# Kernel tuning notes

Hardware: AMD Instinct MI355X
Metric: run time of the kernel (lower is better)

Reference implementation:

```python
import jax, jax.numpy as jnp
import numpy as np

NL, D, Di, N, R, K, V, NH = 24, 768, 1536, 16, 48, 4, 50280, 12
BATCH, SEQ = 4, 256


def setup_inputs():
    key = jax.random.key(0)
    it = iter(jax.random.split(key, 48))
    g = lambda shape, s=0.02: jax.random.normal(next(it), shape, jnp.float32) * s
    inp = {
        "question_ids": jax.random.randint(next(it), (BATCH, SEQ), 0, V),
        "question_mask": jnp.ones((BATCH, SEQ), jnp.int32),
        "answer_ids": jax.random.randint(next(it), (BATCH, SEQ), 0, V),
        "answer_mask": jnp.ones((BATCH, SEQ), jnp.int32),
        "embed": g((V, D)),
        "norm_w": jnp.ones((NL, D)),
        "in_proj_w": g((NL, 2 * Di, D)),
        "conv_w": g((NL, Di, K), 0.1),
        "conv_b": jnp.zeros((NL, Di)),
        "x_proj_w": g((NL, R + 2 * N, Di)),
        "dt_proj_w": g((NL, Di, R)),
        "dt_proj_b": g((NL, Di), 0.5) - 4.0,
        "A_log": jnp.log(jnp.broadcast_to(jnp.arange(1, N + 1, dtype=jnp.float32), (NL, Di, N))) + 0.0,
        "D_p": jnp.ones((NL, Di)),
        "out_proj_w": g((NL, D, Di)),
        "norm_f": jnp.ones((D,)),
        "ln1_w": jnp.ones((D,)), "ln1_b": jnp.zeros((D,)),
        "qkv_w": g((3 * D, D)), "qkv_b": jnp.zeros((3 * D,)),
        "attn_out_w": g((D, D)), "attn_out_b": jnp.zeros((D,)),
        "ln2_w": jnp.ones((D,)), "ln2_b": jnp.zeros((D,)),
        "ff1_w": g((4 * D, D)), "ff1_b": jnp.zeros((4 * D,)),
        "ff2_w": g((D, 4 * D)), "ff2_b": jnp.zeros((D,)),
        "C_w": g((1, N)), "proj_out_w": g((D, Di)),
        "B_w": g((N, 1)), "proj_in_w": g((Di, D), 0.002),
    }
    return inp


def _rms(x, w, eps=1e-5):
    return x * jax.lax.rsqrt(jnp.mean(x * x, axis=-1, keepdims=True) + eps) * w


def _ln(x, w, b, eps=1e-5):
    m = jnp.mean(x, axis=-1, keepdims=True)
    v = jnp.var(x, axis=-1, keepdims=True)
    return (x - m) * jax.lax.rsqrt(v + eps) * w + b


def _mamba_block(h, layer, init_state):
    nw, ipw, cw, cb, xpw, dpw, dpb, alog, dp, opw = layer
    x_in = _rms(h, nw)
    xz = jnp.einsum('bld,ed->ble', x_in, ipw)  # (B,L,2*Di)
    x, z = jnp.split(xz, 2, axis=-1)
    L = x.shape[1]
    xp = jnp.pad(x, ((0, 0), (K - 1, 0), (0, 0)))  # causal depthwise conv, kernel K
    x = sum(xp[:, k:k + L, :] * cw[:, k] for k in range(K)) + cb
    x = jax.nn.silu(x)
    dbl = jnp.einsum('bld,ed->ble', x, xpw)
    dt, Bm, Cm = dbl[..., :R], dbl[..., R:R + N], dbl[..., R + N:]
    delta = jax.nn.softplus(jnp.einsum('blr,dr->bld', dt, dpw) + dpb)  # (B,L,Di)
    A = -jnp.exp(alog)  # (Di,N)

    def step(hs, t):  # selective scan, carry (B,Di,N)
        d_t, x_t, B_t, C_t = t
        hs = jnp.exp(d_t[..., None] * A) * hs + (d_t * x_t)[..., None] * B_t[:, None, :]
        return hs, jnp.einsum('bdn,bn->bd', hs, C_t)

    xs = tuple(jnp.moveaxis(a, 1, 0) for a in (delta, x, Bm, Cm))
    last, ys = jax.lax.scan(step, init_state, xs)
    y = jnp.moveaxis(ys, 0, 1) + x * dp
    y = y * jax.nn.silu(z)
    return h + jnp.einsum('bld,od->blo', y, opw), last


def _backbone(ids, mask, embed, mamba_params, norm_f, init_states):
    h = embed[ids] * mask[..., None].astype(embed.dtype)
    block = jax.checkpoint(_mamba_block)  # remat per layer: bounds bwd memory

    def layer_step(carry, xs):
        *layer, st = xs
        return block(carry, tuple(layer), st)

    h, lasts = jax.lax.scan(layer_step, h, mamba_params + (init_states,))
    h = _rms(h, norm_f)
    return jnp.einsum('bld,vd->blv', h, embed), lasts  # tied lm head


def _tf_layer(x, ln1_w, ln1_b, qkv_w, qkv_b, attn_out_w, attn_out_b, ln2_w, ln2_b, ff1_w, ff1_b, ff2_w, ff2_b):
    B, S, _ = x.shape
    hd = D // NH
    y = _ln(x, ln1_w, ln1_b)  # norm_first pre-LN
    q, k, v = jnp.split(y @ qkv_w.T + qkv_b, 3, axis=-1)
    q = q.reshape(B, S, NH, hd); k = k.reshape(B, S, NH, hd); v = v.reshape(B, S, NH, hd)
    att = jax.nn.softmax(jnp.einsum('bqhd,bkhd->bhqk', q, k) / jnp.sqrt(jnp.float32(hd)), axis=-1)
    o = jnp.einsum('bhqk,bkhd->bqhd', att, v).reshape(B, S, D)
    x = x + o @ attn_out_w.T + attn_out_b
    y = _ln(x, ln2_w, ln2_b)
    return x + jax.nn.gelu(y @ ff1_w.T + ff1_b, approximate=False) @ ff2_w.T + ff2_b


def _refine(states, C_w, proj_out_w, B_w, proj_in_w, tf_params):
    # states: (B, NL, Di, N); 12-step recurrent state refinement
    for _ in range(12):
        d = jnp.einsum('bsdn,n->bsd', states, C_w[0])  # C: Linear(16,1), squeeze(-1)
        d = jnp.einsum('bsd,od->bso', d, proj_out_w)   # 1536 -> 768
        d = _tf_layer(d, *tf_params)
        d = jnp.einsum('bso,do->bsd', d, proj_in_w)    # 768 -> 1536
        states = states + d[..., None] * B_w[:, 0]     # B: Linear(1,16)
    return states


def reference(question_ids, question_mask, answer_ids, answer_mask, embed, norm_w, in_proj_w, conv_w, conv_b, x_proj_w, dt_proj_w, dt_proj_b, A_log, D_p, out_proj_w, norm_f, ln1_w, ln1_b, qkv_w, qkv_b, attn_out_w, attn_out_b, ln2_w, ln2_b, ff1_w, ff1_b, ff2_w, ff2_b, C_w, proj_out_w, B_w, proj_in_w):
    mamba_params = (norm_w, in_proj_w, conv_w, conv_b, x_proj_w, dt_proj_w, dt_proj_b, A_log, D_p, out_proj_w)
    tf_params = (ln1_w, ln1_b, qkv_w, qkv_b, attn_out_w, attn_out_b, ln2_w, ln2_b, ff1_w, ff1_b, ff2_w, ff2_b)
    Bsz = question_ids.shape[0]
    zeros = jnp.zeros((NL, Bsz, Di, N), embed.dtype)
    _, lasts = _backbone(question_ids, question_mask, embed, mamba_params, norm_f, zeros)
    states = jnp.moveaxis(lasts, 0, 1)  # torch.stack(states, dim=1): (B, NL, Di, N)
    states = _refine(states, C_w, proj_out_w, B_w, proj_in_w, tf_params)
    logits, _ = _backbone(answer_ids, answer_mask, embed, mamba_params, norm_f, jnp.moveaxis(states, 0, 1))
    return logits
```

## Files before the change

### kernel.cpp

```cpp
#include <hip/hip_runtime.h>
#include <math.h>

namespace {

constexpr int kNL = 24, kD = 768, kDi = 1536, kN = 16, kR = 48, kK = 4, kV = 50280, kNH = 12;
constexpr int kB = 4, kS = 256;
constexpr int kMtok = kB * kS;
constexpr int kMref = kB * kNL;
constexpr int kVp = 50304;
constexpr int kKa = 3840;

using bf16x8   = __attribute__((ext_vector_type(8))) short;
using f32x4    = __attribute__((ext_vector_type(4))) float;
using ushort8v = __attribute__((ext_vector_type(8))) unsigned short;

__device__ __forceinline__ float siluf(float x) { return x / (1.f + __expf(-x)); }

__device__ __forceinline__ ushort f2b(float f) {
    union { float f; unsigned u; } v; v.f = f;
    unsigned u = v.u;
    unsigned r = (u + 0x7FFFu + ((u >> 16) & 1u)) >> 16;
    return (ushort)r;
}
__device__ __forceinline__ float b2f(ushort u) {
    union { unsigned u; float f; } v; v.u = (unsigned)u << 16; return v.f;
}

#define GLOAD_LDS(g, l) \
    __builtin_amdgcn_global_load_lds((const __attribute__((address_space(1))) void*)(g), \
                                     (__attribute__((address_space(3))) void*)(l), 16, 0, 0)

template <int BM, int BN, int BIAS, int ACT, int RES, int OUTMODE, int PIPE, int SSQ = 0>
__global__ __launch_bounds__(256, (PIPE == 3 ? 3 : 2)) void gemm_bf16(
    const ushort* __restrict__ A, int lda,
    const ushort* __restrict__ B, int ldb,
    float* __restrict__ C, int ldc,
    ushort* __restrict__ Cbf, int ldcb,
    float* __restrict__ C2,
    const float* __restrict__ bias,
    const float* __restrict__ aux,
    const float* __restrict__ aux2,
    int M, int N, int K)
{
    constexpr int ACH = BM / 32;
    constexpr int BCH = BN / 32;
    constexpr int MI  = BM / 32;
    constexpr int NJ  = BN / 32;

    __shared__ ushort As[PIPE][BM * 64];
    __shared__ ushort Bs[PIPE][BN * 64];

    const int tid  = threadIdx.x;
    const int lane = tid & 63;
    const int wave = tid >> 6;
    const int m0 = blockIdx.y * BM;
    const int n0 = blockIdx.x * BN;
    const int wr = (wave >> 1) * (BM / 2);
    const int wc = (wave & 1) * (BN / 2);

    f32x4 acc[MI][NJ];
#pragma unroll
    for (int i = 0; i < MI; ++i)
#pragma unroll
        for (int j = 0; j < NJ; ++j) acc[i][j] = f32x4{0.f, 0.f, 0.f, 0.f};

    const int srow = lane >> 3;
    const int scol = ((lane & 7) ^ srow) * 8;
    const ushort* gA[ACH];
    const ushort* gB[BCH];
#pragma unroll
    for (int g = 0; g < ACH; ++g)
        gA[g] = A + (size_t)(m0 + (g * 4 + wave) * 8 + srow) * lda + scol;
#pragma unroll
    for (int g = 0; g < BCH; ++g)
        gB[g] = B + (size_t)(n0 + (g * 4 + wave) * 8 + srow) * ldb + scol;

    const int frow = lane & 15;
    const int kh   = lane >> 4;
    const int nt   = K >> 6;

    auto stage = [&](int t, int buf) {
        const int off = t * 64;
#pragma unroll
        for (int g = 0; g < ACH; ++g) GLOAD_LDS(gA[g] + off, &As[buf][(g * 4 + wave) * 512]);
#pragma unroll
        for (int g = 0; g < BCH; ++g) GLOAD_LDS(gB[g] + off, &Bs[buf][(g * 4 + wave) * 512]);
    };
    auto compute = [&](int buf) {
#pragma unroll
        for (int s = 0; s < 2; ++s) {
            bf16x8 fa[MI], fb[NJ];
#pragma unroll
            for (int i = 0; i < MI; ++i) {
                int r = wr + i * 16 + frow;
                int slot = (s * 4 + kh) ^ (r & 7);
                fa[i] = *(const bf16x8*)&As[buf][r * 64 + slot * 8];
            }
#pragma unroll
            for (int j = 0; j < NJ; ++j) {
                int r = wc + j * 16 + frow;
                int slot = (s * 4 + kh) ^ (r & 7);
                fb[j] = *(const bf16x8*)&Bs[buf][r * 64 + slot * 8];
            }
#pragma unroll
            for (int i = 0; i < MI; ++i)
#pragma unroll
                for (int j = 0; j < NJ; ++j)
                    acc[i][j] = __builtin_amdgcn_mfma_f32_16x16x32_bf16(fa[i], fb[j], acc[i][j], 0, 0, 0);
        }
    };

    if constexpr (PIPE == 3) {
        stage(0, 0);
        if (nt > 1) stage(1, 1);
        for (int t = 0; t < nt; ++t) {
            if (t < nt - 1) {
                asm volatile("s_waitcnt vmcnt(%0)" :: "n"(ACH + BCH) : "memory");
            } else {
                asm volatile("s_waitcnt vmcnt(0)" ::: "memory");
            }
            __builtin_amdgcn_s_barrier();
            if (t + 2 < nt) stage(t + 2, (t + 2) % 3);
            compute(t % 3);
        }
        __builtin_amdgcn_s_barrier();
    } else {
        stage(0, 0);
        __syncthreads();
        int cur = 0;
        for (int t = 0; t < nt; ++t) {
            if (t + 1 < nt) stage(t + 1, cur ^ 1);
            compute(cur);
            __syncthreads();
            cur ^= 1;
        }
    }

    const int ccol = lane & 15;
    const int crow = (lane >> 4) * 4;
    float rsq[MI][4], rsm[MI][4];
    if constexpr (SSQ) {
#pragma unroll
        for (int i = 0; i < MI; ++i)
#pragma unroll
            for (int q = 0; q < 4; ++q) { rsq[i][q] = 0.f; rsm[i][q] = 0.f; }
    }
#pragma unroll
    for (int i = 0; i < MI; ++i) {
#pragma unroll
        for (int j = 0; j < NJ; ++j) {
            int gn = n0 + wc + j * 16 + ccol;
            if (gn >= N) continue;
            float bv = BIAS ? bias[gn] : 0.f;
#pragma unroll
            for (int q = 0; q < 4; ++q) {
                int gm = m0 + wr + i * 16 + crow + q;
                if (gm >= M) continue;
                float v = acc[i][j][q] + bv;
                if (ACT == 1) v = fmaxf(v, 0.f) + log1pf(expf(-fabsf(v)));
                if (ACT == 2) v = 0.5f * v * (1.f + erff(v * 0.70710678118654752f));
                if (OUTMODE == 3) {
                    if (gn < 48) Cbf[(size_t)gm * 64 + gn] = f2b(v);
                    else if (gn < 64) { Cbf[(size_t)gm * 64 + gn] = 0; C2[(size_t)(gn - 48) * kMtok + gm] = v; }
                    else if (gn < 80) C2[(size_t)(gn - 48) * kMtok + gm] = v;
                } else if (OUTMODE == 4) {
                    ((ushort*)C2)[(size_t)gn * kMtok + gm] = f2b(v);
                } else if (OUTMODE == 7) {
                    int bb = gm / kNL, ss = gm - bb * kNL;
                    float* stp = C2 + ((size_t)(ss * kB + bb) * kDi + gn) * kN;
                    float a2 = 0.f;
#pragma unroll
                    for (int nn = 0; nn < kN; ++nn) {
                        float sv = stp[nn] + v * aux2[nn];
                        stp[nn] = sv;
                        a2 += sv * aux[nn];
                    }
                    Cbf[(size_t)gm * ldcb + gn] = f2b(a2);
                } else {
                    size_t ci = (size_t)gm * ldc + gn;
                    if (RES) v += C[ci];
                    if (OUTMODE != 2) C[ci] = v;
                    if (OUTMODE == 1 || OUTMODE == 2) Cbf[(size_t)gm * ldcb + gn] = f2b(v);
                    if constexpr (SSQ) { rsq[i][q] += v * v; rsm[i][q] += v; }
                }
            }
        }
    }
    if constexpr (SSQ) {
#pragma unroll
        for (int i = 0; i < MI; ++i)
#pragma unroll
            for (int q = 0; q < 4; ++q) {
                rsq[i][q] += __shfl_xor(rsq[i][q], 1, 16);
                rsq[i][q] += __shfl_xor(rsq[i][q], 2, 16);
                rsq[i][q] += __shfl_xor(rsq[i][q], 4, 16);
                rsq[i][q] += __shfl_xor(rsq[i][q], 8, 16);
                if (SSQ == 2) {
                    rsm[i][q] += __shfl_xor(rsm[i][q], 1, 16);
                    rsm[i][q] += __shfl_xor(rsm[i][q], 2, 16);
                    rsm[i][q] += __shfl_xor(rsm[i][q], 4, 16);
                    rsm[i][q] += __shfl_xor(rsm[i][q], 8, 16);
                }
            }
        float* red = (float*)&As[0][0];
        __syncthreads();
        if ((lane & 15) == 0) {
#pragma unroll
            for (int i = 0; i < MI; ++i)
#pragma unroll
                for (int q = 0; q < 4; ++q) {
                    int rl = (wave >> 1) * (BM / 2) + i * 16 + (lane >> 4) * 4 + q;
                    red[(wave & 1) * BM + rl] = rsq[i][q];
                    if (SSQ == 2) red[2 * BM + (wave & 1) * BM + rl] = rsm[i][q];
                }
        }
        __syncthreads();
        if (tid < BM) {
            if (SSQ == 1) {
                C2[(size_t)blockIdx.x * kMtok + m0 + tid] = red[tid] + red[BM + tid];
            } else {
                C2[(size_t)blockIdx.x * 128 + m0 + tid] = red[tid] + red[BM + tid];
                C2[(size_t)gridDim.x * 128 + blockIdx.x * 128 + m0 + tid] =
                    red[2 * BM + tid] + red[3 * BM + tid];
            }
        }
    }
}

template <int BM, int BN, int BIAS, int ACT, int RES, int OUTMODE, int PIPE, int SSQ = 0>
static void gemm(const ushort* A, int lda, const ushort* B, int ldb,
                 float* C, int ldc, ushort* Cb, int ldcb, float* C2,
                 const float* bias, const float* aux, int M, int N, int K, hipStream_t s,
                 const float* aux2 = nullptr)
{
    dim3 g((N + BN - 1) / BN, (M + BM - 1) / BM);
    gemm_bf16<BM, BN, BIAS, ACT, RES, OUTMODE, PIPE, SSQ><<<g, dim3(256), 0, s>>>(
        A, lda, B, ldb, C, ldc, Cb, ldcb, C2, bias, aux, aux2, M, N, K);
}

__global__ __launch_bounds__(256, 4) void gemm_rms(
    const float* __restrict__ hbuf, const float* __restrict__ ssq,
    const float* __restrict__ nw,
    const ushort* __restrict__ B, int ldb,
    ushort* __restrict__ Xbf, ushort* __restrict__ zTb,
    int M, int N, int K)
{
    constexpr int MI = 2, NJ = 2, BCH = 2;
    __shared__ ushort As[2][64 * 64];
    __shared__ ushort Bs[2][64 * 64];
    const int tid  = threadIdx.x;
    const int lane = tid & 63;
    const int wave = tid >> 6;
    const int m0 = blockIdx.y * 64;
    const int n0 = blockIdx.x * 64;
    const int wr = (wave >> 1) * 32;
    const int wc = (wave & 1) * 32;

    f32x4 acc[MI][NJ];
#pragma unroll
    for (int i = 0; i < MI; ++i)
#pragma unroll
        for (int j = 0; j < NJ; ++j) acc[i][j] = f32x4{0.f, 0.f, 0.f, 0.f};

    const int srow = lane >> 3;
    const int scol = ((lane & 7) ^ srow) * 8;
    const ushort* gB[BCH];
#pragma unroll
    for (int g = 0; g < BCH; ++g)
        gB[g] = B + (size_t)(n0 + (g * 4 + wave) * 8 + srow) * ldb + scol;

    int arow[2];
    float rs[2];
#pragma unroll
    for (int g = 0; g < 2; ++g) {
        arow[g] = m0 + (g * 4 + wave) * 8 + srow;
        float s = 0.f;
#pragma unroll
        for (int c = 0; c < 12; ++c) s += ssq[c * kMtok + arow[g]];
        rs[g] = rsqrtf(s * (1.f / 768.f) + 1e-5f);
    }

    const int frow = lane & 15;
    const int kh   = lane >> 4;
    const int nt   = K >> 6;

    float4 av[2][2], wv[2];
    auto loadA = [&](int t) {
        int k = t * 64 + scol;
        wv[0] = *(const float4*)&nw[k];
        wv[1] = *(const float4*)&nw[k + 4];
#pragma unroll
        for (int g = 0; g < 2; ++g) {
            av[g][0] = *(const float4*)&hbuf[(size_t)arow[g] * K + k];
            av[g][1] = *(const float4*)&hbuf[(size_t)arow[g] * K + k + 4];
        }
    };
    auto writeA = [&](int buf) {
#pragma unroll
        for (int g = 0; g < 2; ++g) {
            ushort8v o;
            o[0] = f2b(av[g][0].x * rs[g] * wv[0].x);
            o[1] = f2b(av[g][0].y * rs[g] * wv[0].y);
            o[2] = f2b(av[g][0].z * rs[g] * wv[0].z);
            o[3] = f2b(av[g][0].w * rs[g] * wv[0].w);
            o[4] = f2b(av[g][1].x * rs[g] * wv[1].x);
            o[5] = f2b(av[g][1].y * rs[g] * wv[1].y);
            o[6] = f2b(av[g][1].z * rs[g] * wv[1].z);
            o[7] = f2b(av[g][1].w * rs[g] * wv[1].w);
            *(ushort8v*)&As[buf][(g * 4 + wave) * 512 + lane * 8] = o;
        }
    };
    auto stageB = [&](int t, int buf) {
#pragma unroll
        for (int g = 0; g < BCH; ++g) GLOAD_LDS(gB[g] + t * 64, &Bs[buf][(g * 4 + wave) * 512]);
    };
    auto compute = [&](int buf) {
#pragma unroll
        for (int s = 0; s < 2; ++s) {
            bf16x8 fa[MI], fb[NJ];
#pragma unroll
            for (int i = 0; i < MI; ++i) {
                int r = wr + i * 16 + frow;
                int slot = (s * 4 + kh) ^ (r & 7);
                fa[i] = *(const bf16x8*)&As[buf][r * 64 + slot * 8];
            }
#pragma unroll
            for (int j = 0; j < NJ; ++j) {
                int r = wc + j * 16 + frow;
                int slot = (s * 4 + kh) ^ (r & 7);
                fb[j] = *(const bf16x8*)&Bs[buf][r * 64 + slot * 8];
            }
#pragma unroll
            for (int i = 0; i < MI; ++i)
#pragma unroll
                for (int j = 0; j < NJ; ++j)
                    acc[i][j] = __builtin_amdgcn_mfma_f32_16x16x32_bf16(fa[i], fb[j], acc[i][j], 0, 0, 0);
        }
    };

    loadA(0);
    stageB(0, 0);
    writeA(0);
    __syncthreads();
    int cur = 0;
    for (int t = 0; t < nt; ++t) {
        if (t + 1 < nt) { loadA(t + 1); stageB(t + 1, cur ^ 1); }
        compute(cur);
        if (t + 1 < nt) writeA(cur ^ 1);
        __syncthreads();
        cur ^= 1;
    }

    const int ccol = lane & 15;
    const int crow = (lane >> 4) * 4;
#pragma unroll
    for (int i = 0; i < MI; ++i) {
#pragma unroll
        for (int j = 0; j < NJ; ++j) {
            int gn = n0 + wc + j * 16 + ccol;
#pragma unroll
            for (int q = 0; q < 4; ++q) {
                int gm = m0 + wr + i * 16 + crow + q;
                float v = acc[i][j][q];
                if (gn < kDi) Xbf[(size_t)gm * kDi + gn] = f2b(v);
                else zTb[(size_t)(gn - kDi) * kMtok + gm] = f2b(siluf(v));
            }
        }
    }
}

template <int ACT, int OUTBF>
__global__ __launch_bounds__(256, 4) void gemm_ln(
    const float* __restrict__ hbuf, const float* __restrict__ pp,
    const float* __restrict__ lw, const float* __restrict__ lb,
    const ushort* __restrict__ B, int ldb,
    float* __restrict__ C, int ldc,
    ushort* __restrict__ Cbf, int ldcb,
    const float* __restrict__ bias,
    int M, int N, int K)
{
    constexpr int MI = 2, NJ = 2, BCH = 2, NP = 12;
    __shared__ ushort As[2][64 * 64];
    __shared__ ushort Bs[2][64 * 64];
    const int tid  = threadIdx.x;
    const int lane = tid & 63;
    const int wave = tid >> 6;
    const int m0 = blockIdx.y * 64;
    const int n0 = blockIdx.x * 64;
    const int wr = (wave >> 1) * 32;
    const int wc = (wave & 1) * 32;

    f32x4 acc[MI][NJ];
#pragma unroll
    for (int i = 0; i < MI; ++i)
#pragma unroll
        for (int j = 0; j < NJ; ++j) acc[i][j] = f32x4{0.f, 0.f, 0.f, 0.f};

    const int srow = lane >> 3;
    const int scol = ((lane & 7) ^ srow) * 8;
    const ushort* gB[BCH];
#pragma unroll
    for (int g = 0; g < BCH; ++g)
        gB[g] = B + (size_t)(n0 + (g * 4 + wave) * 8 + srow) * ldb + scol;

    int arow[2];
    float mean[2], rsv[2];
#pragma unroll
    for (int g = 0; g < 2; ++g) {
        arow[g] = m0 + (g * 4 + wave) * 8 + srow;
        float sq = 0.f, sm = 0.f;
#pragma unroll
        for (int c = 0; c < NP; ++c) {
            sq += pp[c * 128 + arow[g]];
            sm += pp[NP * 128 + c * 128 + arow[g]];
        }
        float mu = sm * (1.f / 768.f);
        mean[g] = mu;
        rsv[g] = rsqrtf(sq * (1.f / 768.f) - mu * mu + 1e-5f);
    }

    const int frow = lane & 15;
    const int kh   = lane >> 4;
    const int nt   = K >> 6;

    float4 av[2][2], wv[2], bv2[2];
    auto loadA = [&](int t) {
        int k = t * 64 + scol;
        wv[0]  = *(const float4*)&lw[k];
        wv[1]  = *(const float4*)&lw[k + 4];
        bv2[0] = *(const float4*)&lb[k];
        bv2[1] = *(const float4*)&lb[k + 4];
#pragma unroll
        for (int g = 0; g < 2; ++g) {
            av[g][0] = *(const float4*)&hbuf[(size_t)arow[g] * K + k];
            av[g][1] = *(const float4*)&hbuf[(size_t)arow[g] * K + k + 4];
        }
    };
    auto writeA = [&](int buf) {
#pragma unroll
        for (int g = 0; g < 2; ++g) {
            ushort8v o;
            o[0] = f2b((av[g][0].x - mean[g]) * rsv[g] * wv[0].x + bv2[0].x);
            o[1] = f2b((av[g][0].y - mean[g]) * rsv[g] * wv[0].y + bv2[0].y);
            o[2] = f2b((av[g][0].z - mean[g]) * rsv[g] * wv[0].z + bv2[0].z);
            o[3] = f2b((av[g][0].w - mean[g]) * rsv[g] * wv[0].w + bv2[0].w);
            o[4] = f2b((av[g][1].x - mean[g]) * rsv[g] * wv[1].x + bv2[1].x);
            o[5] = f2b((av[g][1].y - mean[g]) * rsv[g] * wv[1].y + bv2[1].y);
            o[6] = f2b((av[g][1].z - mean[g]) * rsv[g] * wv[1].z + bv2[1].z);
            o[7] = f2b((av[g][1].w - mean[g]) * rsv[g] * wv[1].w + bv2[1].w);
            *(ushort8v*)&As[buf][(g * 4 + wave) * 512 + lane * 8] = o;
        }
    };
    auto stageB = [&](int t, int buf) {
#pragma unroll
        for (int g = 0; g < BCH; ++g) GLOAD_LDS(gB[g] + t * 64, &Bs[buf][(g * 4 + wave) * 512]);
    };
    auto compute = [&](int buf) {
#pragma unroll
        for (int s = 0; s < 2; ++s) {
            bf16x8 fa[MI], fb[NJ];
#pragma unroll
            for (int i = 0; i < MI; ++i) {
                int r = wr + i * 16 + frow;
                int slot = (s * 4 + kh) ^ (r & 7);
                fa[i] = *(const bf16x8*)&As[buf][r * 64 + slot * 8];
            }
#pragma unroll
            for (int j = 0; j < NJ; ++j) {
                int r = wc + j * 16 + frow;
                int slot = (s * 4 + kh) ^ (r & 7);
                fb[j] = *(const bf16x8*)&Bs[buf][r * 64 + slot * 8];
            }
#pragma unroll
            for (int i = 0; i < MI; ++i)
#pragma unroll
                for (int j = 0; j < NJ; ++j)
                    acc[i][j] = __builtin_amdgcn_mfma_f32_16x16x32_bf16(fa[i], fb[j], acc[i][j], 0, 0, 0);
        }
    };

    loadA(0);
    stageB(0, 0);
    writeA(0);
    __syncthreads();
    int cur = 0;
    for (int t = 0; t < nt; ++t) {
        if (t + 1 < nt) { loadA(t + 1); stageB(t + 1, cur ^ 1); }
        compute(cur);
        if (t + 1 < nt) writeA(cur ^ 1);
        __syncthreads();
        cur ^= 1;
    }

    const int ccol = lane & 15;
    const int crow = (lane >> 4) * 4;
#pragma unroll
    for (int i = 0; i < MI; ++i) {
#pragma unroll
        for (int j = 0; j < NJ; ++j) {
            int gn = n0 + wc + j * 16 + ccol;
            if (gn >= N) continue;
            float bvv = bias[gn];
#pragma unroll
            for (int q = 0; q < 4; ++q) {
                int gm = m0 + wr + i * 16 + crow + q;
                if (gm >= M) continue;
                float v = acc[i][j][q] + bvv;
                if (ACT == 2) v = 0.5f * v * (1.f + erff(v * 0.70710678118654752f));
                if (OUTBF) Cbf[(size_t)gm * ldcb + gn] = f2b(v);
                else       C[(size_t)gm * ldc + gn] = v;
            }
        }
    }
}

__global__ void cvt_kernel(const float* __restrict__ src, ushort* __restrict__ dst, int n) {
    int i = (blockIdx.x * 256 + threadIdx.x) * 4;
    if (i >= n) return;
    float4 v = *(const float4*)(src + i);
    ushort4 o; o.x = f2b(v.x); o.y = f2b(v.y); o.z = f2b(v.z); o.w = f2b(v.w);
    *(ushort4*)(dst + i) = o;
}

__global__ void cvt_xpw_kernel(const float* __restrict__ src, ushort* __restrict__ dst) {
    int i = (blockIdx.x * 256 + threadIdx.x) * 4;
    if (i >= 24 * 80 * 1536) return;
    int l = i / (80 * 1536), r = i - l * (80 * 1536);
    int row = r / 1536, col = r - row * 1536;
    float4 v = *(const float4*)(src + i);
    ushort4 o; o.x = f2b(v.x); o.y = f2b(v.y); o.z = f2b(v.z); o.w = f2b(v.w);
    *(ushort4*)(dst + ((size_t)(l * 128 + row)) * 1536 + col) = o;
}

__global__ void cvt_dpw_kernel(const float* __restrict__ src, ushort* __restrict__ dst) {
    int i = blockIdx.x * 256 + threadIdx.x;
    if (i >= 24 * 1536 * 64) return;
    int col = i & 63, row = i >> 6;
    dst[i] = (col < 48) ? f2b(src[(size_t)row * 48 + col]) : (ushort)0;
}

__global__ void cvt_ff2T_kernel(const float* __restrict__ src, ushort* __restrict__ dst) {
    int i = blockIdx.x * 256 + threadIdx.x;
    if (i >= 768 * 3072) return;
    int d = i / 3072, f = i - d * 3072;
    dst[(size_t)f * 768 + d] = f2b(src[i]);
}

__global__ void cvt_pi_kernel(const float* __restrict__ src, ushort* __restrict__ dst) {
    int i = blockIdx.x * 256 + threadIdx.x;
    if (i >= 1536 * 768) return;
    int o = i / 768, d = i - o * 768;
    dst[(size_t)o * kKa + d] = f2b(src[i]);
}

__global__ void pib_kernel(const float* __restrict__ piw, const float* __restrict__ ff2b,
                           float* __restrict__ bias2) {
    int o = blockIdx.x * 256 + threadIdx.x;
    if (o >= 1536) return;
    float s = 0.f;
    for (int d = 0; d < 768; ++d) s += piw[(size_t)o * 768 + d] * ff2b[d];
    bias2[o] = s;
}

__global__ void embed_kernel(const int* __restrict__ ids, const int* __restrict__ msk,
                             const float* __restrict__ embed, float* __restrict__ h,
                             float* __restrict__ ssq)
{
    int i = blockIdx.x * 256 + threadIdx.x;
    int row = i / kD, col = i - row * kD;
    float v = embed[(size_t)ids[row] * kD + col] * (float)msk[row];
    h[i] = v;
    float s = v * v;
    s += __shfl_xor(s, 1);  s += __shfl_xor(s, 2);  s += __shfl_xor(s, 4);
    s += __shfl_xor(s, 8);  s += __shfl_xor(s, 16); s += __shfl_xor(s, 32);
    if ((threadIdx.x & 63) == 0) ssq[(col >> 6) * kMtok + row] = s;
}

__global__ __launch_bounds__(256) void rms_kernel(const float* __restrict__ x,
                                                  const float* __restrict__ w,
                                                  ushort* __restrict__ out)
{
    __shared__ float red[256];
    int row = blockIdx.x, tid = threadIdx.x;
    const float* xr = x + (size_t)row * kD;
    float s = 0.f;
    for (int j = tid; j < kD; j += 256) { float v = xr[j]; s += v * v; }
    red[tid] = s; __syncthreads();
    for (int o = 128; o > 0; o >>= 1) { if (tid < o) red[tid] += red[tid + o]; __syncthreads(); }
    float rs = rsqrtf(red[0] / (float)kD + 1e-5f);
    for (int j = tid; j < kD; j += 256) out[(size_t)row * kD + j] = f2b(xr[j] * rs * w[j]);
}

__global__ __launch_bounds__(256) void conv_kernel(
    const ushort* __restrict__ xb, const float* __restrict__ cw,
    const float* __restrict__ cb, ushort* __restrict__ xc_bf,
    ushort* __restrict__ xcT)
{
    int d   = blockIdx.x * 256 + threadIdx.x;
    int bt0 = blockIdx.y * 16;
    int t0  = bt0 & (kS - 1);
    float w0 = cw[d * 4], w1 = cw[d * 4 + 1], w2 = cw[d * 4 + 2], w3 = cw[d * 4 + 3];
    float bias = cb[d];
    float xv[19];
#pragma unroll
    for (int j = 0; j < 19; ++j) {
        int tt = t0 - 3 + j;
        xv[j] = (tt >= 0) ? b2f(xb[(size_t)(bt0 - 3 + j) * kDi + d]) : 0.f;
    }
    ushort8v o0, o1;
#pragma unroll
    for (int e = 0; e < 16; ++e) {
        float s = bias + xv[e] * w0 + xv[e + 1] * w1 + xv[e + 2] * w2 + xv[e + 3] * w3;
        ushort us = f2b(siluf(s));
        xc_bf[(size_t)(bt0 + e) * kDi + d] = us;
        if (e < 8) o0[e] = us; else o1[e - 8] = us;
    }
    *(ushort8v*)(xcT + (size_t)d * kMtok + bt0)     = o0;
    *(ushort8v*)(xcT + (size_t)d * kMtok + bt0 + 8) = o1;
}

__global__ __launch_bounds__(256) void scan_kernel(
    const ushort* __restrict__ dltT, const ushort* __restrict__ xcT,
    const ushort* __restrict__ zT, const float* __restrict__ bcT,
    const float* __restrict__ alog, const float* __restrict__ dp,
    float* __restrict__ states, ushort* __restrict__ y)
{
    int gid = blockIdx.x * 256 + threadIdx.x;
    int n = gid & 15;
    int d = (gid >> 4) % kDi;
    int b = gid / (kDi * kN);
    float Areg = -__expf(alog[d * kN + n]);
    float dpv = dp[d];
    size_t sidx = (size_t)(b * kDi + d) * kN + n;
    float hs = states[sidx];
    const ushort8v* pD = (const ushort8v*)(dltT + (size_t)d * kMtok + b * kS);
    const ushort8v* pX = (const ushort8v*)(xcT  + (size_t)d * kMtok + b * kS);
    const ushort8v* pZ = (const ushort8v*)(zT   + (size_t)d * kMtok + b * kS);
    const float4* pB = (const float4*)(bcT + (size_t)n * kMtok + b * kS);
    const float4* pC = (const float4*)(bcT + (size_t)(16 + n) * kMtok + b * kS);
    ushort8v D = pD[0], X = pX[0], Z = pZ[0];
    float4 B0 = pB[0], B1 = pB[1], C0 = pC[0], C1 = pC[1];
    ushort* yrow = y + (size_t)(b * kS) * kDi + d;
    for (int g = 0; g < kS / 8; ++g) {
        ushort8v Dn, Xn, Zn; float4 Bn0, Bn1, Cn0, Cn1;
        if (g + 1 < kS / 8) {
            Dn = pD[g + 1]; Xn = pX[g + 1]; Zn = pZ[g + 1];
            Bn0 = pB[2 * g + 2]; Bn1 = pB[2 * g + 3];
            Cn0 = pC[2 * g + 2]; Cn1 = pC[2 * g + 3];
        }
#pragma unroll
        for (int e = 0; e < 8; ++e) {
            float dv = b2f(D[e]), xv = b2f(X[e]), zv = b2f(Z[e]);
            float Bv = (e < 4) ? (&B0.x)[e] : (&B1.x)[e - 4];
            float Cv = (e < 4) ? (&C0.x)[e] : (&C1.x)[e - 4];
            hs = __expf(dv * Areg) * hs + (dv * xv) * Bv;
            float p = hs * Cv;
            p += __shfl_xor(p, 1, 16);
            p += __shfl_xor(p, 2, 16);
            p += __shfl_xor(p, 4, 16);
            p += __shfl_xor(p, 8, 16);
            if (n == 0) yrow[(size_t)(g * 8 + e) * kDi] = f2b((p + xv * dpv) * zv);
        }
        D = Dn; X = Xn; Z = Zn; B0 = Bn0; B1 = Bn1; C0 = Cn0; C1 = Cn1;
    }
    states[sidx] = hs;
}

__global__ void contract_kernel(const float* __restrict__ st, const float* __restrict__ Cw,
                                ushort* __restrict__ dDi)
{
    int i = blockIdx.x * 256 + threadIdx.x;
    int row = i / kDi, di = i - row * kDi;
    int b = row / kNL, s = row - b * kNL;
    const float* sp = st + ((size_t)(s * kB + b) * kDi + di) * kN;
    float acc = 0.f;
#pragma unroll
    for (int nn = 0; nn < kN; ++nn) acc += sp[nn] * Cw[nn];
    dDi[i] = f2b(acc);
}

__global__ __launch_bounds__(32) void attn_kernel(const float* __restrict__ qkv,
                                                  ushort* __restrict__ o)
{
    int b = blockIdx.x / kNH;
    int hh = blockIdx.x - b * kNH;
    int sq = threadIdx.x;
    if (sq >= kNL) return;
    const float* qrow = qkv + (size_t)(b * kNL + sq) * (3 * kD) + hh * 64;
    float q[64];
#pragma unroll
    for (int e = 0; e < 64; ++e) q[e] = qrow[e];
    float sc[kNL];
    float mx = -1e30f;
    for (int sk = 0; sk < kNL; ++sk) {
        const float* krow = qkv + (size_t)(b * kNL + sk) * (3 * kD) + kD + hh * 64;
        float dt = 0.f;
#pragma unroll
        for (int e = 0; e < 64; ++e) dt += q[e] * krow[e];
        dt *= 0.125f;
        sc[sk] = dt;
        mx = fmaxf(mx, dt);
    }
    float sum = 0.f;
    for (int sk = 0; sk < kNL; ++sk) { sc[sk] = expf(sc[sk] - mx); sum += sc[sk]; }
    float inv = 1.f / sum;
    float out[64];
#pragma unroll
    for (int e = 0; e < 64; ++e) out[e] = 0.f;
    for (int sk = 0; sk < kNL; ++sk) {
        float wgt = sc[sk] * inv;
        const float* vrow = qkv + (size_t)(b * kNL + sk) * (3 * kD) + 2 * kD + hh * 64;
#pragma unroll
        for (int e = 0; e < 64; ++e) out[e] += wgt * vrow[e];
    }
    ushort* orow = o + (size_t)(b * kNL + sq) * kD + hh * 64;
#pragma unroll
    for (int e = 0; e < 64; ++e) orow[e] = f2b(out[e]);
}

}

extern "C" void kernel_launch(void* const* d_in, const int* in_sizes, int n_in,
                              void* d_out, int out_size, void* d_ws, size_t ws_size,
                              hipStream_t stream)
{
    const int*   q_ids  = (const int*)d_in[0];
    const int*   q_msk  = (const int*)d_in[1];
    const int*   a_ids  = (const int*)d_in[2];
    const int*   a_msk  = (const int*)d_in[3];
    const float* embed  = (const float*)d_in[4];
    const float* norm_w = (const float*)d_in[5];
    const float* ipw    = (const float*)d_in[6];
    const float* cw     = (const float*)d_in[7];
    const float* cb     = (const float*)d_in[8];
    const float* xpw    = (const float*)d_in[9];
    const float* dpw    = (const float*)d_in[10];
    const float* dpb    = (const float*)d_in[11];
    const float* alog   = (const float*)d_in[12];
    const float* dpp    = (const float*)d_in[13];
    const float* opw    = (const float*)d_in[14];
    const float* norm_f = (const float*)d_in[15];
    const float* ln1w   = (const float*)d_in[16];
    const float* ln1b   = (const float*)d_in[17];
    const float* qkvw   = (const float*)d_in[18];
    const float* qkvbi  = (const float*)d_in[19];
    const float* aow    = (const float*)d_in[20];
    const float* aob    = (const float*)d_in[21];
    const float* ln2w   = (const float*)d_in[22];
    const float* ln2b   = (const float*)d_in[23];
    const float* ff1w   = (const float*)d_in[24];
    const float* ff1b   = (const float*)d_in[25];
    const float* ff2w   = (const float*)d_in[26];
    const float* ff2b   = (const float*)d_in[27];
    const float* Cwp    = (const float*)d_in[28];
    const float* powp   = (const float*)d_in[29];
    const float* Bwp    = (const float*)d_in[30];
    const float* piwp   = (const float*)d_in[31];

    char* base = (char*)d_ws;
    size_t cur = 0;
    auto allocB = [&](size_t bytes) { char* p = base + cur; cur = (cur + bytes + 255) & ~(size_t)255; return p; };
    auto allocF = [&](size_t n) { return (float*)allocB(n * 4); };
    auto allocH = [&](size_t n) { return (ushort*)allocB(n * 2); };

    float* h     = allocF((size_t)kMtok * kD);
    float* ssqp  = allocF((size_t)12 * kMtok);
    float* bcT   = allocF((size_t)32 * kMtok);
    float* st    = allocF((size_t)kNL * kB * kDi * kN);
    float* x768  = allocF((size_t)128 * kD);
    float* qkvB  = allocF((size_t)128 * 3 * kD);
    float* bias2 = allocF((size_t)kDi);
    float* pp1   = allocF((size_t)2 * 12 * 128);
    float* pp2   = allocF((size_t)2 * 12 * 128);
    ushort* x_bf    = allocH((size_t)kMtok * kDi);
    ushort* zT_b    = allocH((size_t)kDi * kMtok);
    ushort* xcT_b   = allocH((size_t)kDi * kMtok);
    ushort* dltT_b  = allocH((size_t)kDi * kMtok);
    ushort* xc_bf   = allocH((size_t)kMtok * kDi);
    ushort* dtin_bf = allocH((size_t)kMtok * 64);
    ushort* yb_bf   = allocH((size_t)kMtok * kDi);
    ushort* xin_bf  = allocH((size_t)kMtok * kD);
    ushort* dDi_bf  = allocH((size_t)128 * kDi);
    ushort* o768_bf = allocH((size_t)128 * kD);
    ushort* A2      = allocH((size_t)128 * kKa);
    ushort* xpw_bf  = allocH((size_t)kNL * 128 * kDi);
    ushort* dpw_bf  = allocH((size_t)kNL * kDi * 64);
    ushort* powp_bf = allocH((size_t)kD * kDi);
    ushort* qkvw_bf = allocH((size_t)3 * kD * kD);
    ushort* aow_bf  = allocH((size_t)kD * kD);
    ushort* ff1w_bf = allocH((size_t)4 * kD * kD);
    ushort* ff2wT   = allocH((size_t)4 * kD * kD);
    ushort* piw_bf  = allocH((size_t)kDi * kD);
    ushort* B2      = allocH((size_t)kDi * kKa);
    ushort* emb_bf  = allocH((size_t)kVp * kD);

    size_t base_end = cur;
    ushort* ipw_all = allocH((size_t)kNL * 2 * kDi * kD);
    ushort* opw_all = allocH((size_t)kNL * kD * kDi);
    bool full = (cur <= ws_size);
    ushort* ipw_stg = nullptr;
    ushort* opw_stg = nullptr;
    if (!full) {
        cur = base_end;
        ipw_stg = allocH((size_t)2 * kDi * kD);
        opw_stg = allocH((size_t)kD * kDi);
        if (cur > ws_size) return;
    }

    auto cvt = [&](const float* s, ushort* d, size_t n) {
        cvt_kernel<<<dim3((unsigned)((n / 4 + 255) / 256)), dim3(256), 0, stream>>>(s, d, (int)n);
    };

    hipMemsetAsync(st, 0, sizeof(float) * (size_t)kNL * kB * kDi * kN, stream);

    cvt_xpw_kernel<<<dim3(2880), dim3(256), 0, stream>>>(xpw, xpw_bf);
    cvt_dpw_kernel<<<dim3(9216), dim3(256), 0, stream>>>(dpw, dpw_bf);
    cvt(powp, powp_bf, (size_t)kD * kDi);
    cvt(qkvw, qkvw_bf, (size_t)3 * kD * kD);
    cvt(aow,  aow_bf,  (size_t)kD * kD);
    cvt(ff1w, ff1w_bf, (size_t)4 * kD * kD);
    cvt(piwp, piw_bf,  (size_t)kDi * kD);
    cvt_ff2T_kernel<<<dim3(9216), dim3(256), 0, stream>>>(ff2w, ff2wT);
    cvt_pi_kernel<<<dim3(4608), dim3(256), 0, stream>>>(piwp, B2);
    pib_kernel<<<dim3(6), dim3(256), 0, stream>>>(piwp, ff2b, bias2);
    gemm<64, 64, 0, 0, 0, 2, 3>(piw_bf, kD, ff2wT, kD, nullptr, 0, B2 + kD, kKa, nullptr,
                                nullptr, nullptr, kDi, 4 * kD, kD, stream);
    cvt(embed, emb_bf, (size_t)kV * kD);
    if (full) {
        cvt(ipw, ipw_all, (size_t)kNL * 2 * kDi * kD);
        cvt(opw, opw_all, (size_t)kNL * kD * kDi);
    }

    for (int pass = 0; pass < 2; ++pass) {
        const int* ids = pass ? a_ids : q_ids;
        const int* msk = pass ? a_msk : q_msk;

        embed_kernel<<<dim3(kMtok * kD / 256), dim3(256), 0, stream>>>(ids, msk, embed, h, ssqp);

        for (int l = 0; l < kNL; ++l) {
            const ushort* ipw_l;
            const ushort* opw_l;
            if (full) {
                ipw_l = ipw_all + (size_t)l * 2 * kDi * kD;
                opw_l = opw_all + (size_t)l * kD * kDi;
            } else {
                cvt(ipw + (size_t)l * 2 * kDi * kD, ipw_stg, (size_t)2 * kDi * kD);
                cvt(opw + (size_t)l * kD * kDi, opw_stg, (size_t)kD * kDi);
                ipw_l = ipw_stg;
                opw_l = opw_stg;
            }
            gemm_rms<<<dim3(48, 16), dim3(256), 0, stream>>>(
                h, ssqp, norm_w + (size_t)l * kD, ipw_l, kD, x_bf, zT_b, kMtok, 2 * kDi, kD);
            conv_kernel<<<dim3(kDi / 256, kMtok / 16), dim3(256), 0, stream>>>(
                x_bf, cw + (size_t)l * kDi * kK, cb + (size_t)l * kDi, xc_bf, xcT_b);
            gemm<64, 64, 0, 0, 0, 3, 3>(xc_bf, kDi, xpw_bf + (size_t)l * 128 * kDi, kDi,
                                        nullptr, 0, dtin_bf, 0, bcT,
                                        nullptr, nullptr, kMtok, 128, kDi, stream);
            gemm<64, 64, 1, 1, 0, 4, 3>(dtin_bf, 64, dpw_bf + (size_t)l * kDi * 64, 64,
                                        nullptr, 0, nullptr, 0, (float*)dltT_b,
                                        dpb + (size_t)l * kDi, nullptr, kMtok, kDi, 64, stream);
            scan_kernel<<<dim3(kB * kDi * kN / 256), dim3(256), 0, stream>>>(
                dltT_b, xcT_b, zT_b, bcT, alog + (size_t)l * kDi * kN, dpp + (size_t)l * kDi,
                st + (size_t)l * kB * kDi * kN, yb_bf);
            gemm<64, 64, 0, 0, 1, 0, 3, 1>(yb_bf, kDi, opw_l, kDi, h, kD, nullptr, 0, ssqp,
                                           nullptr, nullptr, kMtok, kD, kDi, stream);
        }

        if (pass == 0) {
            contract_kernel<<<dim3(kMref * kDi / 256), dim3(256), 0, stream>>>(st, Cwp, dDi_bf);
            for (int it = 0; it < 12; ++it) {
                gemm<64, 64, 0, 0, 0, 0, 3, 2>(dDi_bf, kDi, powp_bf, kDi, x768, kD, nullptr, 0, pp1,
                                               nullptr, nullptr, kMref, kD, kDi, stream);
                gemm_ln<0, 0><<<dim3(36, 2), dim3(256), 0, stream>>>(
                    x768, pp1, ln1w, ln1b, qkvw_bf, kD, qkvB, 3 * kD, nullptr, 0, qkvbi,
                    kMref, 3 * kD, kD);
                attn_kernel<<<dim3(kB * kNH), dim3(32), 0, stream>>>(qkvB, o768_bf);
                gemm<64, 64, 1, 0, 1, 1, 3, 2>(o768_bf, kD, aow_bf, kD, x768, kD, A2, kKa, pp2,
                                               aob, nullptr, kMref, kD, kD, stream);
                gemm_ln<2, 1><<<dim3(48, 2), dim3(256), 0, stream>>>(
                    x768, pp2, ln2w, ln2b, ff1w_bf, kD, nullptr, 0, A2 + kD, kKa, ff1b,
                    kMref, 4 * kD, kD);
                gemm<64, 64, 1, 0, 0, 7, 3>(A2, kKa, B2, kKa, nullptr, 0, dDi_bf, kDi, st,
                                            bias2, Cwp, kMref, kDi, kKa, stream, Bwp);
            }
        } else {
            rms_kernel<<<dim3(kMtok), dim3(256), 0, stream>>>(h, norm_f, xin_bf);
            gemm<128, 128, 0, 0, 0, 0, 2>(xin_bf, kD, emb_bf, kD, (float*)d_out, kV, nullptr, 0, nullptr,
                                          nullptr, nullptr, kMtok, kV, kD, stream);
        }
    }
}
```

Before: 8.727 ms.

## Fuse causal conv into x_proj GEMM and scan, drop conv kernel

```diff
diff --git a/kernel.cpp b/kernel.cpp
--- a/kernel.cpp
+++ b/kernel.cpp
@@ -159,11 +159,7 @@
                 float v = acc[i][j][q] + bv;
                 if (ACT == 1) v = fmaxf(v, 0.f) + log1pf(expf(-fabsf(v)));
                 if (ACT == 2) v = 0.5f * v * (1.f + erff(v * 0.70710678118654752f));
-                if (OUTMODE == 3) {
-                    if (gn < 48) Cbf[(size_t)gm * 64 + gn] = f2b(v);
-                    else if (gn < 64) { Cbf[(size_t)gm * 64 + gn] = 0; C2[(size_t)(gn - 48) * kMtok + gm] = v; }
-                    else if (gn < 80) C2[(size_t)(gn - 48) * kMtok + gm] = v;
-                } else if (OUTMODE == 4) {
+                if (OUTMODE == 4) {
                     ((ushort*)C2)[(size_t)gn * kMtok + gm] = f2b(v);
                 } else if (OUTMODE == 7) {
                     int bb = gm / kNL, ss = gm - bb * kNL;
@@ -242,7 +238,7 @@
     const float* __restrict__ hbuf, const float* __restrict__ ssq,
     const float* __restrict__ nw,
     const ushort* __restrict__ B, int ldb,
-    ushort* __restrict__ Xbf, ushort* __restrict__ zTb,
+    ushort* __restrict__ Xbf, ushort* __restrict__ xTb, ushort* __restrict__ zTb,
     int M, int N, int K)
 {
     constexpr int MI = 2, NJ = 2, BCH = 2;
@@ -362,8 +358,157 @@
             for (int q = 0; q < 4; ++q) {
                 int gm = m0 + wr + i * 16 + crow + q;
                 float v = acc[i][j][q];
-                if (gn < kDi) Xbf[(size_t)gm * kDi + gn] = f2b(v);
-                else zTb[(size_t)(gn - kDi) * kMtok + gm] = f2b(siluf(v));
+                if (gn < kDi) {
+                    ushort uv = f2b(v);
+                    Xbf[(size_t)gm * kDi + gn] = uv;
+                    xTb[(size_t)gn * kMtok + gm] = uv;
+                } else {
+                    zTb[(size_t)(gn - kDi) * kMtok + gm] = f2b(siluf(v));
+                }
+            }
+        }
+    }
+}
+
+__global__ __launch_bounds__(256, 2) void gemm_conv(
+    const ushort* __restrict__ xb,
+    const float* __restrict__ cw,
+    const float* __restrict__ cb,
+    const ushort* __restrict__ B, int ldb,
+    ushort* __restrict__ dtin,
+    float* __restrict__ bcT,
+    int M, int N, int K)
+{
+    constexpr int MI = 2, NJ = 2, BCH = 2;
+    __shared__ ushort As[2][64 * 64];
+    __shared__ ushort Bs[2][64 * 64];
+    const int tid  = threadIdx.x;
+    const int lane = tid & 63;
+    const int wave = tid >> 6;
+    const int m0 = blockIdx.y * 64;
+    const int n0 = blockIdx.x * 64;
+    const int wr = (wave >> 1) * 32;
+    const int wc = (wave & 1) * 32;
+
+    f32x4 acc[MI][NJ];
+#pragma unroll
+    for (int i = 0; i < MI; ++i)
+#pragma unroll
+        for (int j = 0; j < NJ; ++j) acc[i][j] = f32x4{0.f, 0.f, 0.f, 0.f};
+
+    const int srow = lane >> 3;
+    const int scol = ((lane & 7) ^ srow) * 8;
+    const ushort* gB[BCH];
+#pragma unroll
+    for (int g = 0; g < BCH; ++g)
+        gB[g] = B + (size_t)(n0 + (g * 4 + wave) * 8 + srow) * ldb + scol;
+
+    int arow[2], tloc[2];
+#pragma unroll
+    for (int g = 0; g < 2; ++g) {
+        arow[g] = m0 + (g * 4 + wave) * 8 + srow;
+        tloc[g] = arow[g] & (kS - 1);
+    }
+
+    const int frow = lane & 15;
+    const int kh   = lane >> 4;
+    const int nt   = K >> 6;
+
+    ushort8v xr4[2][4];
+    float4 w4[8];
+    float cbv[8];
+    auto loadA = [&](int t) {
+        int k = t * 64 + scol;
+#pragma unroll
+        for (int e = 0; e < 8; ++e) w4[e] = *(const float4*)&cw[(size_t)(k + e) * 4];
+        float4 c0 = *(const float4*)&cb[k];
+        float4 c1 = *(const float4*)&cb[k + 4];
+        cbv[0] = c0.x; cbv[1] = c0.y; cbv[2] = c0.z; cbv[3] = c0.w;
+        cbv[4] = c1.x; cbv[5] = c1.y; cbv[6] = c1.z; cbv[7] = c1.w;
+#pragma unroll
+        for (int g = 0; g < 2; ++g) {
+#pragma unroll
+            for (int j = 0; j < 4; ++j) {
+                if (tloc[g] - 3 + j >= 0) {
+                    xr4[g][j] = *(const ushort8v*)&xb[(size_t)(arow[g] - 3 + j) * kDi + k];
+                } else {
+                    ushort8v z;
+#pragma unroll
+                    for (int e = 0; e < 8; ++e) z[e] = 0;
+                    xr4[g][j] = z;
+                }
+            }
+        }
+    };
+    auto writeA = [&](int buf) {
+#pragma unroll
+        for (int g = 0; g < 2; ++g) {
+            ushort8v o;
+#pragma unroll
+            for (int e = 0; e < 8; ++e) {
+                float s = cbv[e] + b2f(xr4[g][0][e]) * w4[e].x + b2f(xr4[g][1][e]) * w4[e].y
+                                 + b2f(xr4[g][2][e]) * w4[e].z + b2f(xr4[g][3][e]) * w4[e].w;
+                o[e] = f2b(siluf(s));
+            }
+            *(ushort8v*)&As[buf][(g * 4 + wave) * 512 + lane * 8] = o;
+        }
+    };
+    auto stageB = [&](int t, int buf) {
+#pragma unroll
+        for (int g = 0; g < BCH; ++g) GLOAD_LDS(gB[g] + t * 64, &Bs[buf][(g * 4 + wave) * 512]);
+    };
+    auto compute = [&](int buf) {
+#pragma unroll
+        for (int s = 0; s < 2; ++s) {
+            bf16x8 fa[MI], fb[NJ];
+#pragma unroll
+            for (int i = 0; i < MI; ++i) {
+                int r = wr + i * 16 + frow;
+                int slot = (s * 4 + kh) ^ (r & 7);
+                fa[i] = *(const bf16x8*)&As[buf][r * 64 + slot * 8];
+            }
+#pragma unroll
+            for (int j = 0; j < NJ; ++j) {
+                int r = wc + j * 16 + frow;
+                int slot = (s * 4 + kh) ^ (r & 7);
+                fb[j] = *(const bf16x8*)&Bs[buf][r * 64 + slot * 8];
+            }
+#pragma unroll
+            for (int i = 0; i < MI; ++i)
+#pragma unroll
+                for (int j = 0; j < NJ; ++j)
+                    acc[i][j] = __builtin_amdgcn_mfma_f32_16x16x32_bf16(fa[i], fb[j], acc[i][j], 0, 0, 0);
+        }
+    };
+
+    loadA(0);
+    stageB(0, 0);
+    writeA(0);
+    __syncthreads();
+    int cur = 0;
+    for (int t = 0; t < nt; ++t) {
+        if (t + 1 < nt) { loadA(t + 1); stageB(t + 1, cur ^ 1); }
+        compute(cur);
+        if (t + 1 < nt) writeA(cur ^ 1);
+        __syncthreads();
+        cur ^= 1;
+    }
+
+    const int ccol = lane & 15;
+    const int crow = (lane >> 4) * 4;
+#pragma unroll
+    for (int i = 0; i < MI; ++i) {
+#pragma unroll
+        for (int j = 0; j < NJ; ++j) {
+            int gn = n0 + wc + j * 16 + ccol;
+            if (gn >= 80) continue;
+#pragma unroll
+            for (int q = 0; q < 4; ++q) {
+                int gm = m0 + wr + i * 16 + crow + q;
+                float v = acc[i][j][q];
+                if (gn < 48) dtin[(size_t)gm * 64 + gn] = f2b(v);
+                else if (gn < 64) { dtin[(size_t)gm * 64 + gn] = 0; bcT[(size_t)(gn - 48) * kMtok + gm] = v; }
+                else bcT[(size_t)(gn - 48) * kMtok + gm] = v;
             }
         }
     }
@@ -591,38 +736,11 @@
     for (int j = tid; j < kD; j += 256) out[(size_t)row * kD + j] = f2b(xr[j] * rs * w[j]);
 }
 
-__global__ __launch_bounds__(256) void conv_kernel(
-    const ushort* __restrict__ xb, const float* __restrict__ cw,
-    const float* __restrict__ cb, ushort* __restrict__ xc_bf,
-    ushort* __restrict__ xcT)
-{
-    int d   = blockIdx.x * 256 + threadIdx.x;
-    int bt0 = blockIdx.y * 16;
-    int t0  = bt0 & (kS - 1);
-    float w0 = cw[d * 4], w1 = cw[d * 4 + 1], w2 = cw[d * 4 + 2], w3 = cw[d * 4 + 3];
-    float bias = cb[d];
-    float xv[19];
-#pragma unroll
-    for (int j = 0; j < 19; ++j) {
-        int tt = t0 - 3 + j;
-        xv[j] = (tt >= 0) ? b2f(xb[(size_t)(bt0 - 3 + j) * kDi + d]) : 0.f;
-    }
-    ushort8v o0, o1;
-#pragma unroll
-    for (int e = 0; e < 16; ++e) {
-        float s = bias + xv[e] * w0 + xv[e + 1] * w1 + xv[e + 2] * w2 + xv[e + 3] * w3;
-        ushort us = f2b(siluf(s));
-        xc_bf[(size_t)(bt0 + e) * kDi + d] = us;
-        if (e < 8) o0[e] = us; else o1[e - 8] = us;
-    }
-    *(ushort8v*)(xcT + (size_t)d * kMtok + bt0)     = o0;
-    *(ushort8v*)(xcT + (size_t)d * kMtok + bt0 + 8) = o1;
-}
-
 __global__ __launch_bounds__(256) void scan_kernel(
-    const ushort* __restrict__ dltT, const ushort* __restrict__ xcT,
+    const ushort* __restrict__ dltT, const ushort* __restrict__ xT,
     const ushort* __restrict__ zT, const float* __restrict__ bcT,
     const float* __restrict__ alog, const float* __restrict__ dp,
+    const float* __restrict__ cw, const float* __restrict__ cb,
     float* __restrict__ states, ushort* __restrict__ y)
 {
     int gid = blockIdx.x * 256 + threadIdx.x;
@@ -631,15 +749,18 @@
     int b = gid / (kDi * kN);
     float Areg = -__expf(alog[d * kN + n]);
     float dpv = dp[d];
+    float4 wq = *(const float4*)&cw[(size_t)d * 4];
+    float cbv = cb[d];
     size_t sidx = (size_t)(b * kDi + d) * kN + n;
     float hs = states[sidx];
     const ushort8v* pD = (const ushort8v*)(dltT + (size_t)d * kMtok + b * kS);
-    const ushort8v* pX = (const ushort8v*)(xcT  + (size_t)d * kMtok + b * kS);
+    const ushort8v* pX = (const ushort8v*)(xT   + (size_t)d * kMtok + b * kS);
     const ushort8v* pZ = (const ushort8v*)(zT   + (size_t)d * kMtok + b * kS);
     const float4* pB = (const float4*)(bcT + (size_t)n * kMtok + b * kS);
     const float4* pC = (const float4*)(bcT + (size_t)(16 + n) * kMtok + b * kS);
     ushort8v D = pD[0], X = pX[0], Z = pZ[0];
     float4 B0 = pB[0], B1 = pB[1], C0 = pC[0], C1 = pC[1];
+    float xm3 = 0.f, xm2 = 0.f, xm1 = 0.f;
     ushort* yrow = y + (size_t)(b * kS) * kDi + d;
     for (int g = 0; g < kS / 8; ++g) {
         ushort8v Dn, Xn, Zn; float4 Bn0, Bn1, Cn0, Cn1;
@@ -650,7 +771,11 @@
         }
 #pragma unroll
         for (int e = 0; e < 8; ++e) {
-            float dv = b2f(D[e]), xv = b2f(X[e]), zv = b2f(Z[e]);
+            float dv = b2f(D[e]), zv = b2f(Z[e]);
+            float xr = b2f(X[e]);
+            float s = cbv + xm3 * wq.x + xm2 * wq.y + xm1 * wq.z + xr * wq.w;
+            float xv = siluf(s);
+            xm3 = xm2; xm2 = xm1; xm1 = xr;
             float Bv = (e < 4) ? (&B0.x)[e] : (&B1.x)[e - 4];
             float Cv = (e < 4) ? (&C0.x)[e] : (&C1.x)[e - 4];
             hs = __expf(dv * Areg) * hs + (dv * xv) * Bv;
@@ -773,10 +898,9 @@
     float* pp1   = allocF((size_t)2 * 12 * 128);
     float* pp2   = allocF((size_t)2 * 12 * 128);
     ushort* x_bf    = allocH((size_t)kMtok * kDi);
+    ushort* xT_b    = allocH((size_t)kDi * kMtok);
     ushort* zT_b    = allocH((size_t)kDi * kMtok);
-    ushort* xcT_b   = allocH((size_t)kDi * kMtok);
     ushort* dltT_b  = allocH((size_t)kDi * kMtok);
-    ushort* xc_bf   = allocH((size_t)kMtok * kDi);
     ushort* dtin_bf = allocH((size_t)kMtok * 64);
     ushort* yb_bf   = allocH((size_t)kMtok * kDi);
     ushort* xin_bf  = allocH((size_t)kMtok * kD);
@@ -850,20 +974,21 @@
                 opw_l = opw_stg;
             }
             gemm_rms<<<dim3(48, 16), dim3(256), 0, stream>>>(
-                h, ssqp, norm_w + (size_t)l * kD, ipw_l, kD, x_bf, zT_b, kMtok, 2 * kDi, kD);
-            conv_kernel<<<dim3(kDi / 256, kMtok / 16), dim3(256), 0, stream>>>(
-                x_bf, cw + (size_t)l * kDi * kK, cb + (size_t)l * kDi, xc_bf, xcT_b);
-            gemm<64, 64, 0, 0, 0, 3, 3>(xc_bf, kDi, xpw_bf + (size_t)l * 128 * kDi, kDi,
-                                        nullptr, 0, dtin_bf, 0, bcT,
-                                        nullptr, nullptr, kMtok, 128, kDi, stream);
+                h, ssqp, norm_w + (size_t)l * kD, ipw_l, kD, x_bf, xT_b, zT_b, kMtok, 2 * kDi, kD);
+            gemm_conv<<<dim3(2, 16), dim3(256), 0, stream>>>(
+                x_bf, cw + (size_t)l * kDi * kK, cb + (size_t)l * kDi,
+                xpw_bf + (size_t)l * 128 * kDi, kDi, dtin_bf, bcT, kMtok, 128, kDi);
             gemm<64, 64, 1, 1, 0, 4, 3>(dtin_bf, 64, dpw_bf + (size_t)l * kDi * 64, 64,
                                         nullptr, 0, nullptr, 0, (float*)dltT_b,
                                         dpb + (size_t)l * kDi, nullptr, kMtok, kDi, 64, stream);
             scan_kernel<<<dim3(kB * kDi * kN / 256), dim3(256), 0, stream>>>(
-                dltT_b, xcT_b, zT_b, bcT, alog + (size_t)l * kDi * kN, dpp + (size_t)l * kDi,
+                dltT_b, xT_b, zT_b, bcT, alog + (size_t)l * kDi * kN, dpp + (size_t)l * kDi,
+                cw + (size_t)l * kDi * kK, cb + (size_t)l * kDi,
                 st + (size_t)l * kB * kDi * kN, yb_bf);
-            gemm<64, 64, 0, 0, 1, 0, 3, 1>(yb_bf, kDi, opw_l, kDi, h, kD, nullptr, 0, ssqp,
-                                           nullptr, nullptr, kMtok, kD, kDi, stream);
+            if (!(pass == 0 && l == kNL - 1)) {
+                gemm<64, 64, 0, 0, 1, 0, 3, 1>(yb_bf, kDi, opw_l, kDi, h, kD, nullptr, 0, ssqp,
+                                               nullptr, nullptr, kMtok, kD, kDi, stream);
+            }
         }
 
         if (pass == 0) {
```

Measured after the change: 10.82 ms. 1.24x slower.
